# Optimization experiments

Measured on AMD Instinct MI355X. Metric: run time of the kernel, lower is better.

The kernel has to match this reference:

```python
import jax, jax.numpy as jnp
import numpy as np

B, D, R = 8192, 4096, 64
REG_W, REG_C = 0.01, 0.05


def setup_inputs() -> dict:
    key = jax.random.key(0)
    ks = jax.random.split(key, 7)
    return {
        "X": jax.random.normal(ks[0], (B, D), dtype=jnp.float32),
        "U1": jax.random.normal(ks[1], (1, D, R), dtype=jnp.float32),
        "U2": jax.random.normal(ks[2], (2, D, R), dtype=jnp.float32),
        "U3": jax.random.normal(ks[3], (3, D, R), dtype=jnp.float32),
        "C": jax.random.normal(ks[4], (3,), dtype=jnp.float32),
        "beta": jax.random.normal(ks[5], (1,), dtype=jnp.float32),
        "C_sin": jax.random.normal(ks[6], (1,), dtype=jnp.float32),
    }


def reference(X, U1, U2, U3, C, beta, C_sin):
    # term_j(x) = sum_r prod_{i<=j} <x, U_j[i, :, r]>
    result = jnp.broadcast_to(beta[0], (X.shape[0],))
    reg_loss_w = jnp.float32(0.0)
    for j, U in enumerate((U1, U2, U3)):
        dots = jnp.einsum("bd,odr->obr", X, U)      # [order, B, R]
        term = jnp.prod(dots, axis=0).sum(axis=1)   # [B]
        result = result + C[j] * term
        reg_loss_w = reg_loss_w + REG_W * (jnp.abs(U).sum() / U.size)
    sine_term = C_sin[0] * jnp.sin(X).sum(axis=1)
    result = result + sine_term
    reg_loss_c = REG_C * (jnp.abs(C).sum() + jnp.abs(C_sin).sum())
    total_reg = reg_loss_w + reg_loss_c
    return result, total_reg
```

## Files before the change

kernel.cpp:

```cpp
#include <hip/hip_runtime.h>
#include <hip/hip_bf16.h>

typedef float f32x4 __attribute__((ext_vector_type(4)));
typedef short s16x8 __attribute__((ext_vector_type(8)));

#define D_DIM 4096
#define NT 24
#define NSLAB 128
#define BM 32
#define DSTRIDE 388
#define SIN_OFF 49664
#define POOL_BYTES 49920

__device__ __forceinline__ unsigned short f2bf(float f) {
    unsigned u = __float_as_uint(f);
    u += 0x7fffu + ((u >> 16) & 1u);
    return (unsigned short)(u >> 16);
}

__global__ __launch_bounds__(64) void reg_init_kernel(const float* __restrict__ C,
                                                      const float* __restrict__ Csin,
                                                      float* __restrict__ reg_out) {
    if (threadIdx.x == 0)
        reg_out[0] = 0.05f * (fabsf(C[0]) + fabsf(C[1]) + fabsf(C[2]) + fabsf(Csin[0]));
}

__global__ __launch_bounds__(64) void build_w_kernel(const float* __restrict__ U1,
                                                     const float* __restrict__ U2,
                                                     const float* __restrict__ U3,
                                                     unsigned short* __restrict__ W,
                                                     float* __restrict__ reg_out) {
    const int ks = blockIdx.x / NT;
    const int ct = blockIdx.x % NT;
    const int l  = threadIdx.x;
    const int n  = ct * 16 + (l & 15);
    const int kb = ks * 32 + ((l >> 4) << 3);

    const float* src;
    float scale;
    if (n < 64)       { src = U1 + n;                  scale = 0.01f / 262144.f; }
    else if (n < 128) { src = U2 + (n - 64);           scale = 0.01f / 524288.f; }
    else if (n < 192) { src = U2 + 262144 + (n - 128); scale = 0.01f / 524288.f; }
    else if (n < 256) { src = U3 + (n - 192);          scale = 0.01f / 786432.f; }
    else if (n < 320) { src = U3 + 262144 + (n - 256); scale = 0.01f / 786432.f; }
    else              { src = U3 + 524288 + (n - 320); scale = 0.01f / 786432.f; }

    unsigned short h[8];
    float sabs = 0.f;
#pragma unroll
    for (int j = 0; j < 8; ++j) {
        float u = src[(size_t)(kb + j) * 64];
        sabs += fabsf(u);
        h[j] = f2bf(u);
    }
    uint4 pk;
    pk.x = (unsigned)h[0] | ((unsigned)h[1] << 16);
    pk.y = (unsigned)h[2] | ((unsigned)h[3] << 16);
    pk.z = (unsigned)h[4] | ((unsigned)h[5] << 16);
    pk.w = (unsigned)h[6] | ((unsigned)h[7] << 16);
    *(uint4*)(W + ((size_t)blockIdx.x * 64 + l) * 8) = pk;

    sabs *= scale;
#pragma unroll
    for (int off = 32; off >= 1; off >>= 1)
        sabs += __shfl_xor(sabs, off, 64);
    if (l == 0) atomicAdd(reg_out, sabs);
}

__global__ __launch_bounds__(1024) void poly_main_kernel(const float* __restrict__ X,
                                                         const unsigned short* __restrict__ W,
                                                         const float* __restrict__ C,
                                                         const float* __restrict__ beta,
                                                         const float* __restrict__ Csin,
                                                         float* __restrict__ out) {
    __shared__ __align__(16) char pool[POOL_BYTES];

    const int t    = threadIdx.x;
    const int lane = t & 63;
    const int wv   = t >> 6;
    const int kg   = wv >> 3;
    const int cg   = wv & 7;
    const int ct0  = cg * 3;
    const int row0 = blockIdx.x * BM;

    const bool isStage = ((t >> 8) & 1) == 0;
    const int p    = t >> 9;
    const int srow = (t >> 3) & 31;
    const int k4   = (t & 7) << 2;
    const float* xp = X + (size_t)(row0 + srow) * D_DIM + k4;
    const int awfrag = (srow >> 4) * 1024
                     + (((((k4 >> 3) & 3) << 4) | (srow & 15)) * 16) + ((k4 & 7) << 1);

    const s16x8* __restrict__ Wf = (const s16x8*)W;

    f32x4 acc00{}, acc01{}, acc02{}, acc10{}, acc11{}, acc12{};
    float sinacc = 0.f;
    f32x4 xcur{};

    if (isStage) {
        f32x4 x0 = *(const f32x4*)(xp + (size_t)p * 32);
        sinacc += __sinf(x0.x) + __sinf(x0.y) + __sinf(x0.z) + __sinf(x0.w);
        short4 h;
        h.x = (short)f2bf(x0.x); h.y = (short)f2bf(x0.y);
        h.z = (short)f2bf(x0.z); h.w = (short)f2bf(x0.w);
        *(short4*)(pool + p * 2048 + awfrag) = h;
        xcur = *(const f32x4*)(xp + (size_t)(2 + p) * 32);
    }
    s16x8 bA0 = Wf[((size_t)kg * NT + ct0 + 0) * 64 + lane];
    s16x8 bA1 = Wf[((size_t)kg * NT + ct0 + 1) * 64 + lane];
    s16x8 bA2 = Wf[((size_t)kg * NT + ct0 + 2) * 64 + lane];
    s16x8 bB0{}, bB1{}, bB2{};
    asm volatile("s_waitcnt lgkmcnt(0)" ::: "memory");
    __builtin_amdgcn_s_barrier();
    __builtin_amdgcn_sched_barrier(0);

#define STAGE(d_)                                                               \
    if (isStage) {                                                              \
        const int sw_ = 2 * (d_) + 2 + p;                                       \
        if (sw_ < NSLAB) {                                                      \
            sinacc += __sinf(xcur.x) + __sinf(xcur.y)                           \
                    + __sinf(xcur.z) + __sinf(xcur.w);                          \
            short4 h_;                                                          \
            h_.x = (short)f2bf(xcur.x); h_.y = (short)f2bf(xcur.y);             \
            h_.z = (short)f2bf(xcur.z); h_.w = (short)f2bf(xcur.w);             \
            *(short4*)(pool + (sw_ & 3) * 2048 + awfrag) = h_;                  \
        }                                                                       \
        int sl_ = 2 * (d_) + 4 + p; if (sl_ > NSLAB - 1) sl_ = NSLAB - 1;       \
        xcur = *(const f32x4*)(xp + (size_t)sl_ * 32);                          \
    }

#define BODY(d_, U0, U1, U2, P0, P1, P2)                                        \
    {                                                                           \
        STAGE(d_);                                                              \
        const int ab_ = ((2 * (d_) + kg) & 3) * 2048;                           \
        s16x8 af0_ = *(const s16x8*)(pool + ab_ + lane * 16);                   \
        s16x8 af1_ = *(const s16x8*)(pool + ab_ + 1024 + lane * 16);            \
        acc00 = __builtin_amdgcn_mfma_f32_16x16x32_bf16(af0_, U0, acc00, 0, 0, 0); \
        acc01 = __builtin_amdgcn_mfma_f32_16x16x32_bf16(af0_, U1, acc01, 0, 0, 0); \
        acc02 = __builtin_amdgcn_mfma_f32_16x16x32_bf16(af0_, U2, acc02, 0, 0, 0); \
        acc10 = __builtin_amdgcn_mfma_f32_16x16x32_bf16(af1_, U0, acc10, 0, 0, 0); \
        acc11 = __builtin_amdgcn_mfma_f32_16x16x32_bf16(af1_, U1, acc11, 0, 0, 0); \
        acc12 = __builtin_amdgcn_mfma_f32_16x16x32_bf16(af1_, U2, acc12, 0, 0, 0); \
        int sp_ = 2 * (d_) + 2 + kg; if (sp_ > NSLAB - 1) sp_ = NSLAB - 1;      \
        P0 = Wf[((size_t)sp_ * NT + ct0 + 0) * 64 + lane];                      \
        P1 = Wf[((size_t)sp_ * NT + ct0 + 1) * 64 + lane];                      \
        P2 = Wf[((size_t)sp_ * NT + ct0 + 2) * 64 + lane];                      \
        asm volatile("s_waitcnt lgkmcnt(0)" ::: "memory");                      \
        __builtin_amdgcn_s_barrier();                                           \
        __builtin_amdgcn_sched_barrier(0);                                      \
    }

    for (int e = 0; e < 32; ++e) {
        BODY(2 * e,     bA0, bA1, bA2, bB0, bB1, bB2);
        BODY(2 * e + 1, bB0, bB1, bB2, bA0, bA1, bA2);
    }
#undef BODY
#undef STAGE

    float* Dm = (float*)pool;
    float* sinpart = (float*)(pool + SIN_OFF);
    const f32x4 accA[2][3] = {{acc00, acc01, acc02}, {acc10, acc11, acc12}};
    const int lr4 = (lane >> 4) << 2;
    const int lc  = lane & 15;

    if (kg == 0) {
#pragma unroll
        for (int f = 0; f < 2; ++f)
#pragma unroll
            for (int c = 0; c < 3; ++c) {
                const int col = (ct0 + c) * 16 + lc;
#pragma unroll
                for (int i = 0; i < 4; ++i)
                    Dm[(f * 16 + lr4 + i) * DSTRIDE + col] = accA[f][c][i];
            }
    }
    if (isStage) {
        sinacc += __shfl_xor(sinacc, 1);
        sinacc += __shfl_xor(sinacc, 2);
        sinacc += __shfl_xor(sinacc, 4);
        if ((t & 7) == 0) sinpart[p * 32 + srow] = sinacc;
    }
    __syncthreads();
    if (kg == 1) {
#pragma unroll
        for (int f = 0; f < 2; ++f)
#pragma unroll
            for (int c = 0; c < 3; ++c) {
                const int col = (ct0 + c) * 16 + lc;
#pragma unroll
                for (int i = 0; i < 4; ++i)
                    Dm[(f * 16 + lr4 + i) * DSTRIDE + col] += accA[f][c][i];
            }
    }
    __syncthreads();

    if (t < 512) {
        const int crow = t >> 4;
        const int cc   = t & 15;
        float t1 = 0.f, t2 = 0.f, t3 = 0.f;
#pragma unroll
        for (int rr = 0; rr < 64; rr += 16) {
            const int r = rr + cc;
            t1 += Dm[crow * DSTRIDE + r];
            t2 += Dm[crow * DSTRIDE + 64 + r]  * Dm[crow * DSTRIDE + 128 + r];
            t3 += Dm[crow * DSTRIDE + 192 + r] * Dm[crow * DSTRIDE + 256 + r]
                                               * Dm[crow * DSTRIDE + 320 + r];
        }
#pragma unroll
        for (int off = 1; off < 16; off <<= 1) {
            t1 += __shfl_xor(t1, off, 16);
            t2 += __shfl_xor(t2, off, 16);
            t3 += __shfl_xor(t3, off, 16);
        }
        if (cc == 0)
            out[row0 + crow] = beta[0] + C[0] * t1 + C[1] * t2 + C[2] * t3
                             + Csin[0] * (sinpart[crow] + sinpart[32 + crow]);
    }
}

extern "C" void kernel_launch(void* const* d_in, const int* in_sizes, int n_in,
                              void* d_out, int out_size, void* d_ws, size_t ws_size,
                              hipStream_t stream) {
    const float* X   = (const float*)d_in[0];
    const float* U1  = (const float*)d_in[1];
    const float* U2  = (const float*)d_in[2];
    const float* U3  = (const float*)d_in[3];
    const float* Cc  = (const float*)d_in[4];
    const float* bet = (const float*)d_in[5];
    const float* Cs  = (const float*)d_in[6];
    float* out = (float*)d_out;
    unsigned short* W = (unsigned short*)d_ws;

    reg_init_kernel<<<1, 64, 0, stream>>>(Cc, Cs, out + 8192);
    build_w_kernel<<<128 * NT, 64, 0, stream>>>(U1, U2, U3, W, out + 8192);
    poly_main_kernel<<<256, 1024, 0, stream>>>(X, W, Cc, bet, Cs, out);
}
```

Baseline: 94.64 us.

## Deepen global prefetch to three-stage rotation and raise MFMA wave priority

```diff
diff --git a/kernel.cpp b/kernel.cpp
--- a/kernel.cpp
+++ b/kernel.cpp
@@ -95,7 +95,7 @@
 
     f32x4 acc00{}, acc01{}, acc02{}, acc10{}, acc11{}, acc12{};
     float sinacc = 0.f;
-    f32x4 xcur{};
+    f32x4 xw{}, xa{}, xb{};
 
     if (isStage) {
         f32x4 x0 = *(const f32x4*)(xp + (size_t)p * 32);
@@ -104,58 +104,65 @@
         h.x = (short)f2bf(x0.x); h.y = (short)f2bf(x0.y);
         h.z = (short)f2bf(x0.z); h.w = (short)f2bf(x0.w);
         *(short4*)(pool + p * 2048 + awfrag) = h;
-        xcur = *(const f32x4*)(xp + (size_t)(2 + p) * 32);
+        xw = *(const f32x4*)(xp + (size_t)(2 + p) * 32);
+        xa = *(const f32x4*)(xp + (size_t)(4 + p) * 32);
+        xb = *(const f32x4*)(xp + (size_t)(6 + p) * 32);
     }
     s16x8 bA0 = Wf[((size_t)kg * NT + ct0 + 0) * 64 + lane];
     s16x8 bA1 = Wf[((size_t)kg * NT + ct0 + 1) * 64 + lane];
     s16x8 bA2 = Wf[((size_t)kg * NT + ct0 + 2) * 64 + lane];
-    s16x8 bB0{}, bB1{}, bB2{};
+    s16x8 bB0 = Wf[((size_t)(2 + kg) * NT + ct0 + 0) * 64 + lane];
+    s16x8 bB1 = Wf[((size_t)(2 + kg) * NT + ct0 + 1) * 64 + lane];
+    s16x8 bB2 = Wf[((size_t)(2 + kg) * NT + ct0 + 2) * 64 + lane];
+    s16x8 bC0{}, bC1{}, bC2{};
     asm volatile("s_waitcnt lgkmcnt(0)" ::: "memory");
     __builtin_amdgcn_s_barrier();
     __builtin_amdgcn_sched_barrier(0);
 
-#define STAGE(d_)                                                               \
-    if (isStage) {                                                              \
-        const int sw_ = 2 * (d_) + 2 + p;                                       \
-        if (sw_ < NSLAB) {                                                      \
-            sinacc += __sinf(xcur.x) + __sinf(xcur.y)                           \
-                    + __sinf(xcur.z) + __sinf(xcur.w);                          \
-            short4 h_;                                                          \
-            h_.x = (short)f2bf(xcur.x); h_.y = (short)f2bf(xcur.y);             \
-            h_.z = (short)f2bf(xcur.z); h_.w = (short)f2bf(xcur.w);             \
-            *(short4*)(pool + (sw_ & 3) * 2048 + awfrag) = h_;                  \
+#define BODY(d_, U0, U1, U2, P0, P1, P2, XW)                                    \
+    {                                                                           \
+        const int d__ = (d_);                                                   \
+        if (isStage) {                                                          \
+            const int sw_ = 2 * d__ + 2 + p;                                    \
+            if (sw_ < NSLAB) {                                                  \
+                sinacc += __sinf(XW.x) + __sinf(XW.y)                           \
+                        + __sinf(XW.z) + __sinf(XW.w);                          \
+                short4 h_;                                                      \
+                h_.x = (short)f2bf(XW.x); h_.y = (short)f2bf(XW.y);             \
+                h_.z = (short)f2bf(XW.z); h_.w = (short)f2bf(XW.w);             \
+                *(short4*)(pool + (sw_ & 3) * 2048 + awfrag) = h_;              \
+            }                                                                   \
+            int sl_ = 2 * d__ + 8 + p; if (sl_ > NSLAB - 1) sl_ = NSLAB - 1;    \
+            XW = *(const f32x4*)(xp + (size_t)sl_ * 32);                        \
         }                                                                       \
-        int sl_ = 2 * (d_) + 4 + p; if (sl_ > NSLAB - 1) sl_ = NSLAB - 1;       \
-        xcur = *(const f32x4*)(xp + (size_t)sl_ * 32);                          \
-    }
-
-#define BODY(d_, U0, U1, U2, P0, P1, P2)                                        \
-    {                                                                           \
-        STAGE(d_);                                                              \
-        const int ab_ = ((2 * (d_) + kg) & 3) * 2048;                           \
+        int sp_ = 2 * d__ + 4 + kg; if (sp_ > NSLAB - 1) sp_ = NSLAB - 1;       \
+        P0 = Wf[((size_t)sp_ * NT + ct0 + 0) * 64 + lane];                      \
+        P1 = Wf[((size_t)sp_ * NT + ct0 + 1) * 64 + lane];                      \
+        P2 = Wf[((size_t)sp_ * NT + ct0 + 2) * 64 + lane];                      \
+        const int ab_ = ((2 * d__ + kg) & 3) * 2048;                            \
         s16x8 af0_ = *(const s16x8*)(pool + ab_ + lane * 16);                   \
         s16x8 af1_ = *(const s16x8*)(pool + ab_ + 1024 + lane * 16);            \
+        asm volatile("s_waitcnt lgkmcnt(0)" ::: "memory");                      \
+        __builtin_amdgcn_sched_barrier(0);                                      \
+        __builtin_amdgcn_s_setprio(1);                                          \
         acc00 = __builtin_amdgcn_mfma_f32_16x16x32_bf16(af0_, U0, acc00, 0, 0, 0); \
         acc01 = __builtin_amdgcn_mfma_f32_16x16x32_bf16(af0_, U1, acc01, 0, 0, 0); \
         acc02 = __builtin_amdgcn_mfma_f32_16x16x32_bf16(af0_, U2, acc02, 0, 0, 0); \
         acc10 = __builtin_amdgcn_mfma_f32_16x16x32_bf16(af1_, U0, acc10, 0, 0, 0); \
         acc11 = __builtin_amdgcn_mfma_f32_16x16x32_bf16(af1_, U1, acc11, 0, 0, 0); \
         acc12 = __builtin_amdgcn_mfma_f32_16x16x32_bf16(af1_, U2, acc12, 0, 0, 0); \
-        int sp_ = 2 * (d_) + 2 + kg; if (sp_ > NSLAB - 1) sp_ = NSLAB - 1;      \
-        P0 = Wf[((size_t)sp_ * NT + ct0 + 0) * 64 + lane];                      \
-        P1 = Wf[((size_t)sp_ * NT + ct0 + 1) * 64 + lane];                      \
-        P2 = Wf[((size_t)sp_ * NT + ct0 + 2) * 64 + lane];                      \
-        asm volatile("s_waitcnt lgkmcnt(0)" ::: "memory");                      \
+        __builtin_amdgcn_s_setprio(0);                                          \
         __builtin_amdgcn_s_barrier();                                           \
         __builtin_amdgcn_sched_barrier(0);                                      \
     }
 
-    for (int e = 0; e < 32; ++e) {
-        BODY(2 * e,     bA0, bA1, bA2, bB0, bB1, bB2);
-        BODY(2 * e + 1, bB0, bB1, bB2, bA0, bA1, bA2);
-    }
+    for (int e = 0; e < 21; ++e) {
+        BODY(3 * e,     bA0, bA1, bA2, bC0, bC1, bC2, xw);
+        BODY(3 * e + 1, bB0, bB1, bB2, bA0, bA1, bA2, xa);
+        BODY(3 * e + 2, bC0, bC1, bC2, bB0, bB1, bB2, xb);
+    }
+    BODY(63, bA0, bA1, bA2, bC0, bC1, bC2, xw);
 #undef BODY
-#undef STAGE
 
     float* Dm = (float*)pool;
     float* sinpart = (float*)(pool + SIN_OFF);
```

New measurement: 93.43 us. No clear change (-1.3%).
